# Kernel optimization log

Hardware: AMD Instinct MI355X
Metric: run time of the kernel (lower is better)

Reference implementation:

```python
import jax, jax.numpy as jnp
import numpy as np

B, TH, TS, HS, WS = 16, 1024, 1024, 1024, 1024


def setup_inputs() -> dict:
    key = jax.random.key(0)
    k1, k2, k3, k4 = jax.random.split(key, 4)
    h = jax.random.normal(k1, (B, TH, HS), dtype=jnp.float32)
    s = jax.random.normal(k2, (B, TS, WS), dtype=jnp.float32)
    # nn.Linear params: weight [out, in], bias [out]
    Wh = jax.random.normal(k3, (HS, HS), dtype=jnp.float32) * 0.02
    bh = jnp.zeros((HS,), dtype=jnp.float32)
    Ws = jax.random.normal(k4, (HS, WS), dtype=jnp.float32) * 0.02
    bs = jnp.zeros((HS,), dtype=jnp.float32)
    return {"h": h, "s": s, "Wh": Wh, "bh": bh, "Ws": Ws, "bs": bs}


def reference(h, s, Wh, bh, Ws, bs):
    hp = jnp.einsum('bth,oh->bto', h, Wh) + bh          # [B, TH, HS]
    sp = jnp.einsum('btw,ow->bto', s, Ws) + bs          # [B, TS, HS]
    scores = jnp.einsum('bik,bjk->bij', hp, sp)         # [B, TH, TS]
    b, th, _ = scores.shape
    # faithful to torch: flat-chunk into rows of length TH, softmax over dim 1
    sm = jax.nn.softmax(scores.reshape(-1, th), axis=1).reshape(b, -1, th)  # [B, TS, TH]
    res = jnp.matmul(sm, hp)                            # [B, TS, HS]
    return res.reshape(-1, res.shape[-1])               # [B*TS, HS]
```

## Files before the change

kernel.cpp:

```cpp
#include <hip/hip_runtime.h>
#include <hip/hip_bf16.h>
#include <stdint.h>


typedef _Float16 half_t;
typedef __attribute__((ext_vector_type(8))) _Float16 half8;
typedef __attribute__((ext_vector_type(4))) _Float16 half4;
typedef __attribute__((ext_vector_type(4))) float floatx4;

__device__ __forceinline__ void gl2lds16(const void* g, void* l) {
    __builtin_amdgcn_global_load_lds(
        (const __attribute__((address_space(1))) uint32_t*)(uintptr_t)g,
        (__attribute__((address_space(3))) uint32_t*)(uintptr_t)l,
        16, 0, 0);
}

#define PH_MID() do { \
    __builtin_amdgcn_s_barrier(); \
    asm volatile("s_waitcnt lgkmcnt(0)" ::: "memory"); \
    __builtin_amdgcn_sched_barrier(0); } while (0)

#define PH_END() __builtin_amdgcn_s_barrier()

#define QUAD(mq, nq) do { \
    __builtin_amdgcn_s_setprio(1); \
    _Pragma("unroll") for (int mi = 0; mi < 4; ++mi) \
    _Pragma("unroll") for (int ni = 0; ni < 2; ++ni) \
    _Pragma("unroll") for (int ks = 0; ks < 2; ++ks) \
        acc[(mq)*4+mi][(nq)*2+ni] = __builtin_amdgcn_mfma_f32_16x16x32_f16( \
            aF[mi][ks], bF[nq][ni][ks], acc[(mq)*4+mi][(nq)*2+ni], 0, 0, 0); \
    __builtin_amdgcn_s_setprio(0); } while (0)

#define NT16 16

template<int WF32, int WH16, int WH16T>
__global__ __launch_bounds__(512, 2) void gemm256(
    const half_t* __restrict__ A, const half_t* __restrict__ B,
    const float* __restrict__ bias,
    float* __restrict__ Cf, half_t* __restrict__ Ch, half_t* __restrict__ ChT,
    int lda, int ldb, int N,
    long aBatch, long bBatch, long cfBatch, int ldcf)
{
    extern __shared__ char smem[];

    const int tid  = threadIdx.x;
    const int wave = tid >> 6;
    const int lane = tid & 63;
    const int wr = wave >> 2;
    const int wc = wave & 3;
    const int lr = lane & 15, lg = lane >> 4;

    const long batch = blockIdx.z;
    const half_t* Ab = A + batch * aBatch;
    const half_t* Bb = B + batch * bBatch;
    const int row0 = blockIdx.x * 256;
    const int col0 = blockIdx.y * 256;

    floatx4 acc[8][4];
#pragma unroll
    for (int m = 0; m < 8; ++m)
#pragma unroll
        for (int n = 0; n < 4; ++n)
            acc[m][n] = (floatx4){0.f, 0.f, 0.f, 0.f};

    auto stageHalf = [&](int buf, int isA, int half, int kk) {
#pragma unroll
        for (int i = 0; i < 2; ++i) {
            const int off = half * 16384 + i * 8192 + tid * 16;
            const int e = off ^ (((off >> 7) & 7) << 4);
            const int r  = e >> 7;
            const int cb = e & 127;
            const char* g = isA
                ? (const char*)Ab + (long)(row0 + r) * ((long)lda * 2) + (long)kk * 2 + cb
                : (const char*)Bb + (long)(col0 + r) * ((long)ldb * 2) + (long)kk * 2 + cb;
            gl2lds16(g, smem + buf * 65536 + (isA ? 0 : 32768)
                          + half * 16384 + i * 8192 + wave * 1024);
        }
    };
    auto ldA = [&](int buf, int mt, int ks) -> half8 {
        const int row = wr * 128 + mt * 16 + lr;
        const int kp = (ks * 64 + lg * 16) ^ ((row & 7) << 4);
        return *(const half8*)(smem + buf * 65536 + row * 128 + kp);
    };
    auto ldB = [&](int buf, int nt, int ks) -> half8 {
        const int row = wc * 64 + nt * 16 + lr;
        const int kp = (ks * 64 + lg * 16) ^ ((row & 7) << 4);
        return *(const half8*)(smem + buf * 65536 + 32768 + row * 128 + kp);
    };

    stageHalf(0, 0, 0, 0);
    stageHalf(0, 0, 1, 0);
    stageHalf(0, 1, 0, 0);
    stageHalf(0, 1, 1, 0);
    stageHalf(1, 0, 0, 64);
    stageHalf(1, 0, 1, 64);
    asm volatile("s_waitcnt vmcnt(4)" ::: "memory");
    __builtin_amdgcn_s_barrier();
    __builtin_amdgcn_sched_barrier(0);

    half8 aF[4][2];
    half8 bF[2][2][2];

    for (int t = 0; t < NT16; ++t) {
        const int cur = t & 1;

#pragma unroll
        for (int mi = 0; mi < 4; ++mi)
#pragma unroll
            for (int ks = 0; ks < 2; ++ks) aF[mi][ks] = ldA(cur, mi, ks);
#pragma unroll
        for (int ni = 0; ni < 2; ++ni)
#pragma unroll
            for (int ks = 0; ks < 2; ++ks) bF[0][ni][ks] = ldB(cur, ni, ks);
        if (t + 1 < NT16) stageHalf(cur ^ 1, 1, 0, (t + 1) * 64);
        PH_MID();
        QUAD(0, 0);
        PH_END();

#pragma unroll
        for (int ni = 0; ni < 2; ++ni)
#pragma unroll
            for (int ks = 0; ks < 2; ++ks) bF[1][ni][ks] = ldB(cur, 2 + ni, ks);
        if (t + 1 < NT16) stageHalf(cur ^ 1, 1, 1, (t + 1) * 64);
        PH_MID();
        QUAD(0, 1);
        PH_END();

#pragma unroll
        for (int mi = 0; mi < 4; ++mi)
#pragma unroll
            for (int ks = 0; ks < 2; ++ks) aF[mi][ks] = ldA(cur, 4 + mi, ks);
        if (t + 2 < NT16) stageHalf(cur, 0, 0, (t + 2) * 64);
        PH_MID();
        QUAD(1, 1);
        PH_END();

        if (t + 2 < NT16) {
            stageHalf(cur, 0, 1, (t + 2) * 64);
            asm volatile("s_waitcnt vmcnt(4)" ::: "memory");
        } else {
            asm volatile("s_waitcnt vmcnt(0)" ::: "memory");
        }
        PH_MID();
        QUAD(1, 0);
        PH_END();
    }

#pragma unroll
    for (int m = 0; m < 8; ++m) {
        const int gr0 = row0 + wr * 128 + m * 16 + lg * 4;
#pragma unroll
        for (int n = 0; n < 4; ++n) {
            const int gc = col0 + wc * 64 + n * 16 + lr;
            floatx4 v = acc[m][n];
            if (bias) {
                const float b = bias[gc];
                v[0] += b; v[1] += b; v[2] += b; v[3] += b;
            }
            if (WF32) {
                float* p = Cf + batch * cfBatch + (long)gr0 * ldcf + gc;
#pragma unroll
                for (int j = 0; j < 4; ++j) p[(long)j * ldcf] = v[j];
            }
            if (WH16) {
#pragma unroll
                for (int j = 0; j < 4; ++j)
                    Ch[(long)(gr0 + j) * N + gc] = (half_t)v[j];
            }
            if (WH16T) {
                const int b2 = gr0 >> 10;
                const int t0 = gr0 & 1023;
                half4 pk = { (half_t)v[0], (half_t)v[1], (half_t)v[2], (half_t)v[3] };
                *(half4*)&ChT[(long)b2 * 1048576 + (long)gc * 1024 + t0] = pk;
            }
        }
    }
}

__global__ void softmax_inplace(float* __restrict__ S) {
    const long r = blockIdx.x;
    float* row = S + r * 1024;
    const int tid = threadIdx.x;
    const int wave = tid >> 6, lane = tid & 63;

    float4 v = ((const float4*)row)[tid];
    float mx = fmaxf(fmaxf(v.x, v.y), fmaxf(v.z, v.w));
#pragma unroll
    for (int off = 32; off > 0; off >>= 1)
        mx = fmaxf(mx, __shfl_xor(mx, off));
    __shared__ float rmx[4], rsm[4];
    if (lane == 0) rmx[wave] = mx;
    __syncthreads();
    mx = fmaxf(fmaxf(rmx[0], rmx[1]), fmaxf(rmx[2], rmx[3]));

    float e0 = __expf(v.x - mx), e1 = __expf(v.y - mx);
    float e2 = __expf(v.z - mx), e3 = __expf(v.w - mx);
    float s = e0 + e1 + e2 + e3;
#pragma unroll
    for (int off = 32; off > 0; off >>= 1)
        s += __shfl_xor(s, off);
    if (lane == 0) rsm[wave] = s;
    __syncthreads();
    s = rsm[0] + rsm[1] + rsm[2] + rsm[3];

    const float inv = 1.0f / s;
    half4 o = { (half_t)(e0 * inv), (half_t)(e1 * inv), (half_t)(e2 * inv), (half_t)(e3 * inv) };
    ((half4*)((half_t*)S + r * 2048))[tid] = o;
}

__global__ void cvt_f16(const float4* __restrict__ src, half4* __restrict__ dst, int n4) {
    const int stride = gridDim.x * blockDim.x;
    for (int i = blockIdx.x * blockDim.x + threadIdx.x; i < n4; i += stride) {
        float4 v = src[i];
        half4 o = { (half_t)v.x, (half_t)v.y, (half_t)v.z, (half_t)v.w };
        dst[i] = o;
    }
}

extern "C" void kernel_launch(void* const* d_in, const int* in_sizes, int n_in,
                              void* d_out, int out_size, void* d_ws, size_t ws_size,
                              hipStream_t stream) {
    const float* h  = (const float*)d_in[0];
    const float* s  = (const float*)d_in[1];
    const float* Wh = (const float*)d_in[2];
    const float* bh = (const float*)d_in[3];
    const float* Ws = (const float*)d_in[4];
    const float* bs = (const float*)d_in[5];

    const long MB = 16384;
    const long D  = 1024;

    char* w = (char*)d_ws;
    half_t* h16 = (half_t*)w;  w += MB * D * 2;
    half_t* s16 = (half_t*)w;  w += MB * D * 2;
    float*  sc  = (float*)h16;
    half_t* Wh16 = (half_t*)w;  w += D * D * 2;
    half_t* Ws16 = (half_t*)w;  w += D * D * 2;
    half_t* hp16 = (half_t*)w;  w += MB * D * 2;
    half_t* sp16 = (half_t*)w;  w += MB * D * 2;
    half_t* hpT  = (half_t*)w;  w += MB * D * 2;

    hipFuncSetAttribute(reinterpret_cast<const void*>(&gemm256<0,1,1>),
                        hipFuncAttributeMaxDynamicSharedMemorySize, 131072);
    hipFuncSetAttribute(reinterpret_cast<const void*>(&gemm256<0,1,0>),
                        hipFuncAttributeMaxDynamicSharedMemorySize, 131072);
    hipFuncSetAttribute(reinterpret_cast<const void*>(&gemm256<1,0,0>),
                        hipFuncAttributeMaxDynamicSharedMemorySize, 131072);

    cvt_f16<<<512,  256, 0, stream>>>((const float4*)Wh, (half4*)Wh16, (int)(D * D / 4));
    cvt_f16<<<512,  256, 0, stream>>>((const float4*)Ws, (half4*)Ws16, (int)(D * D / 4));
    cvt_f16<<<2048, 256, 0, stream>>>((const float4*)h,  (half4*)h16,  (int)(MB * D / 4));
    cvt_f16<<<2048, 256, 0, stream>>>((const float4*)s,  (half4*)s16,  (int)(MB * D / 4));

    gemm256<0,1,1><<<dim3(64, 4, 1), 512, 131072, stream>>>(
        h16, Wh16, bh, nullptr, hp16, hpT, 1024, 1024, 1024, 0, 0, 0, 0);
    gemm256<0,1,0><<<dim3(64, 4, 1), 512, 131072, stream>>>(
        s16, Ws16, bs, nullptr, sp16, nullptr, 1024, 1024, 1024, 0, 0, 0, 0);
    gemm256<1,0,0><<<dim3(4, 4, 16), 512, 131072, stream>>>(
        hp16, sp16, nullptr, sc, nullptr, nullptr, 1024, 1024, 1024,
        1048576L, 1048576L, 1048576L, 1024);
    softmax_inplace<<<16384, 256, 0, stream>>>(sc);
    gemm256<1,0,0><<<dim3(4, 4, 16), 512, 131072, stream>>>(
        (const half_t*)sc, hpT, nullptr, (float*)d_out, nullptr, nullptr,
        2048, 1024, 1024, 2097152L, 1048576L, 1048576L, 1024);
}
```

Baseline: 237.5 us.

## Prefetch both A and B tiles two stages ahead and precompute global offsets

```diff
diff --git a/kernel.cpp b/kernel.cpp
--- a/kernel.cpp
+++ b/kernel.cpp
@@ -63,18 +63,25 @@
         for (int n = 0; n < 4; ++n)
             acc[m][n] = (floatx4){0.f, 0.f, 0.f, 0.f};
 
-    auto stageHalf = [&](int buf, int isA, int half, int kk) {
+    long aOff[2][2], bOff[2][2];
+#pragma unroll
+    for (int hh = 0; hh < 2; ++hh)
 #pragma unroll
         for (int i = 0; i < 2; ++i) {
-            const int off = half * 16384 + i * 8192 + tid * 16;
+            const int off = hh * 16384 + i * 8192 + tid * 16;
             const int e = off ^ (((off >> 7) & 7) << 4);
-            const int r  = e >> 7;
-            const int cb = e & 127;
-            const char* g = isA
-                ? (const char*)Ab + (long)(row0 + r) * ((long)lda * 2) + (long)kk * 2 + cb
-                : (const char*)Bb + (long)(col0 + r) * ((long)ldb * 2) + (long)kk * 2 + cb;
+            const int r = e >> 7, cb = e & 127;
+            aOff[hh][i] = (long)(row0 + r) * (long)(lda * 2) + cb;
+            bOff[hh][i] = (long)(col0 + r) * (long)(ldb * 2) + cb;
+        }
+
+    auto stageHalf = [&](int buf, int isA, int hh, int kk) {
+#pragma unroll
+        for (int i = 0; i < 2; ++i) {
+            const char* g = (isA ? (const char*)Ab + aOff[hh][i]
+                                 : (const char*)Bb + bOff[hh][i]) + (long)kk * 2;
             gl2lds16(g, smem + buf * 65536 + (isA ? 0 : 32768)
-                          + half * 16384 + i * 8192 + wave * 1024);
+                          + hh * 16384 + i * 8192 + wave * 1024);
         }
     };
     auto ldA = [&](int buf, int mt, int ks) -> half8 {
@@ -88,21 +95,20 @@
         return *(const half8*)(smem + buf * 65536 + 32768 + row * 128 + kp);
     };
 
-    stageHalf(0, 0, 0, 0);
-    stageHalf(0, 0, 1, 0);
-    stageHalf(0, 1, 0, 0);
-    stageHalf(0, 1, 1, 0);
-    stageHalf(1, 0, 0, 64);
-    stageHalf(1, 0, 1, 64);
-    asm volatile("s_waitcnt vmcnt(4)" ::: "memory");
+    stageHalf(0, 0, 0, 0);   stageHalf(0, 0, 1, 0);
+    stageHalf(0, 1, 0, 0);   stageHalf(0, 1, 1, 0);
+    stageHalf(1, 0, 0, 64);  stageHalf(1, 0, 1, 64);
+    stageHalf(1, 1, 0, 64);  stageHalf(1, 1, 1, 64);
+    asm volatile("s_waitcnt vmcnt(8)" ::: "memory");
     __builtin_amdgcn_s_barrier();
-    __builtin_amdgcn_sched_barrier(0);
 
     half8 aF[4][2];
     half8 bF[2][2][2];
 
+#pragma unroll 2
     for (int t = 0; t < NT16; ++t) {
         const int cur = t & 1;
+        const int kk2 = (t + 2) * 64;
 
 #pragma unroll
         for (int mi = 0; mi < 4; ++mi)
@@ -112,7 +118,6 @@
         for (int ni = 0; ni < 2; ++ni)
 #pragma unroll
             for (int ks = 0; ks < 2; ++ks) bF[0][ni][ks] = ldB(cur, ni, ks);
-        if (t + 1 < NT16) stageHalf(cur ^ 1, 1, 0, (t + 1) * 64);
         PH_MID();
         QUAD(0, 0);
         PH_END();
@@ -121,7 +126,6 @@
         for (int ni = 0; ni < 2; ++ni)
 #pragma unroll
             for (int ks = 0; ks < 2; ++ks) bF[1][ni][ks] = ldB(cur, 2 + ni, ks);
-        if (t + 1 < NT16) stageHalf(cur ^ 1, 1, 1, (t + 1) * 64);
         PH_MID();
         QUAD(0, 1);
         PH_END();
@@ -130,14 +134,18 @@
         for (int mi = 0; mi < 4; ++mi)
 #pragma unroll
             for (int ks = 0; ks < 2; ++ks) aF[mi][ks] = ldA(cur, 4 + mi, ks);
-        if (t + 2 < NT16) stageHalf(cur, 0, 0, (t + 2) * 64);
+        if (t + 2 < NT16) {
+            stageHalf(cur, 0, 0, kk2);
+            stageHalf(cur, 0, 1, kk2);
+        }
         PH_MID();
         QUAD(1, 1);
         PH_END();
 
         if (t + 2 < NT16) {
-            stageHalf(cur, 0, 1, (t + 2) * 64);
-            asm volatile("s_waitcnt vmcnt(4)" ::: "memory");
+            stageHalf(cur, 1, 0, kk2);
+            stageHalf(cur, 1, 1, kk2);
+            asm volatile("s_waitcnt vmcnt(8)" ::: "memory");
         } else {
             asm volatile("s_waitcnt vmcnt(0)" ::: "memory");
         }
```

Result: slower. 259.5 us (+9.3%).
